# Kernel tuning notes

Measured on AMD Instinct MI355X. Metric: run time of the kernel, lower is better.

Reference implementation:

```python
import jax, jax.numpy as jnp
import numpy as np

B, L, D, K = 16, 2048, 128, 8192
NUM_RQ_STEPS = 1


def _nearest(residual, codebook):
    # residual: [B,L,D], codebook: [K,D]
    d2 = (
        jnp.sum(residual * residual, axis=-1, keepdims=True)  # [B,L,1]
        - 2.0 * jnp.einsum('bld,kd->blk', residual, codebook)  # [B,L,K]
        + jnp.sum(codebook * codebook, axis=-1)  # [K]
    )
    idx = jnp.argmin(d2, axis=-1)  # [B,L]
    return codebook[idx], idx  # gather: [B,L,D]


def setup_inputs() -> dict:
    key = jax.random.key(0)
    k1, k2 = jax.random.split(key)
    z_e = jax.random.normal(k1, (B, L, D), dtype=jnp.float32)
    codebook = jax.random.normal(k2, (K, D), dtype=jnp.float32)
    return {"z_e": z_e, "codebook": codebook}


def reference(z_e, codebook):
    # apply_codebook(z_e, code_sg=True): codebook is stop-gradiented,
    # residual quantization over NUM_RQ_STEPS, straight-through on output.
    cb = jax.lax.stop_gradient(codebook)
    residual = z_e
    z_q = jnp.zeros_like(z_e)
    idx_list = []
    for _ in range(NUM_RQ_STEPS):
        q, idx = _nearest(residual, cb)
        z_q = z_q + q
        residual = residual - q
        idx_list.append(idx)
    indices = jnp.stack(idx_list, axis=-1)  # [B,L,num_rq_steps]
    # straight-through estimator (code_sg=True): grads flow to z_e, not codebook
    z_q = z_e + jax.lax.stop_gradient(z_q - z_e)
    return z_q, indices
```

## Files before the change

kernel.cpp:

```cpp
#include <hip/hip_runtime.h>


#define M_TOK  32768
#define DIM    128
#define KCODES 8192
#define BM     64
#define NT     (KCODES / 256)
#define MARGIN 0.10f

typedef _Float16 half8v __attribute__((ext_vector_type(8)));
typedef float float4v __attribute__((ext_vector_type(4)));

union H2U { _Float16 h; unsigned short u; };
__device__ __forceinline__ unsigned short f2h_bits(_Float16 h) {
  H2U c; c.h = h; return c.u;
}

#define LOADB(bf, base_off) do {                                     \
    _Pragma("unroll") for (int j_ = 0; j_ < 4; ++j_)                 \
      (bf)[j_] = *(const half8v*)(Bp[j_] + (base_off));              \
  } while (0)

#define CONSUME(kk, bf) do {                                         \
    _Pragma("unroll") for (int i_ = 0; i_ < 4; ++i_)                 \
      _Pragma("unroll") for (int j_ = 0; j_ < 4; ++j_)               \
        acc[i_][j_] = __builtin_amdgcn_mfma_f32_16x16x32_f16(        \
            ahi[kk][i_], (bf)[j_], acc[i_][j_], 0, 0, 0);            \
  } while (0)

#define CNORM_OFF  (KCODES * 256)
#define QCNT_OFF   (CNORM_OFF + KCODES * 4)
#define QTOK_OFF   (QCNT_OFF + 64)
#define KMIN_OFF   (QTOK_OFF + M_TOK * 4)

__global__ __launch_bounds__(256) void prep_kernel(
    const float* __restrict__ cb, unsigned short* __restrict__ Cs,
    float* __restrict__ cnorm, int* __restrict__ qcnt) {
  if (blockIdx.x == 0 && threadIdx.x == 0) *qcnt = 0;
  const int k = blockIdx.x * 4 + (threadIdx.x >> 6);
  const int lane = threadIdx.x & 63;
  const float2 v = ((const float2*)(cb + (size_t)k * DIM))[lane];
  float s = v.x * v.x + v.y * v.y;
  #pragma unroll
  for (int off = 32; off > 0; off >>= 1) s += __shfl_down(s, off);
  if (lane == 0) cnorm[k] = s;
  ushort2 hi;
  hi.x = f2h_bits((_Float16)v.x);
  hi.y = f2h_bits((_Float16)v.y);
  *(ushort2*)(Cs + (size_t)k * 128 + lane * 2) = hi;
}

__global__ __launch_bounds__(256, 2) void vq_mfma_kernel(
    const float* __restrict__ ze, const unsigned short* __restrict__ Cs,
    const float* __restrict__ cnorm, const float* __restrict__ cb,
    int* __restrict__ qcnt, int* __restrict__ qtok,
    unsigned long long* __restrict__ kmin,
    float* __restrict__ out_zq, float* __restrict__ out_idx) {
  __shared__ char lds[16384];
  char* const As = lds;

  const int tid = threadIdx.x;
  const int wn = tid >> 6;
  const int lane = tid & 63;
  const int quad = lane >> 4;
  const int l15 = lane & 15;
  const int m0 = blockIdx.x * BM;

  const char* Bp[4];
  #pragma unroll
  for (int j = 0; j < 4; ++j)
    Bp[j] = (const char*)Cs +
            (size_t)(wn * 64 + j * 16 + l15) * 256 + quad * 16;

  {
    const int r = tid >> 2;
    const int qh = tid & 3;
    const float* zrow = ze + (size_t)(m0 + r) * DIM + qh * 32;
    char* arow = As + r * 256;
    const int rx = r & 7;
    #pragma unroll
    for (int i = 0; i < 8; ++i) {
      const float4 v = *(const float4*)(zrow + i * 4);
      ushort4 hh;
      hh.x = f2h_bits((_Float16)v.x);
      hh.y = f2h_bits((_Float16)v.y);
      hh.z = f2h_bits((_Float16)v.z);
      hh.w = f2h_bits((_Float16)v.w);
      const int c = qh * 32 + i * 4;
      *(ushort4*)(arow + ((((c >> 3) ^ rx) << 4) | ((c & 7) << 1))) = hh;
    }
  }
  __syncthreads();

  half8v ahi[4][4];
  #pragma unroll
  for (int ks = 0; ks < 4; ++ks)
    #pragma unroll
    for (int i = 0; i < 4; ++i) {
      const int m = i * 16 + l15;
      const int kslot = ks * 4 + quad;
      ahi[ks][i] = *(const half8v*)(As + m * 256 + ((kslot ^ (m & 7)) << 4));
    }

  float bestv[16], secv[16], idxv[16];
  #pragma unroll
  for (int s = 0; s < 16; ++s) {
    bestv[s] = -3.4e38f; secv[s] = -3.4e38f; idxv[s] = 0.f;
  }

  half8v bf0[4], bf1[4];
  LOADB(bf0, 0);

  for (int nt = 0; nt < NT; ++nt) {
    const size_t tb = (size_t)nt * 65536;
    float cnv[4];
    #pragma unroll
    for (int j = 0; j < 4; ++j)
      cnv[j] = cnorm[nt * 256 + wn * 64 + j * 16 + l15];

    float4v acc[4][4];
    #pragma unroll
    for (int i = 0; i < 4; ++i)
      #pragma unroll
      for (int j = 0; j < 4; ++j) acc[i][j] = (float4v)0.0f;

    LOADB(bf1, tb + 1 * 64);
    CONSUME(0, bf0);
    LOADB(bf0, tb + 2 * 64);
    CONSUME(1, bf1);
    LOADB(bf1, tb + 3 * 64);
    CONSUME(2, bf0);
    if (nt + 1 < NT) LOADB(bf0, tb + 65536);
    CONSUME(3, bf1);

    #pragma unroll
    for (int j = 0; j < 4; ++j) {
      const float nidx = (float)(nt * 256 + wn * 64 + j * 16 + l15);
      const float cn = cnv[j];
      #pragma unroll
      for (int i = 0; i < 4; ++i)
        #pragma unroll
        for (int rg = 0; rg < 4; ++rg) {
          const float sc = fmaf(-0.5f, cn, acc[i][j][rg]);
          const int slot = i * 4 + rg;
          const bool bt = sc > bestv[slot];
          secv[slot] = __builtin_amdgcn_fmed3f(sc, bestv[slot], secv[slot]);
          idxv[slot] = bt ? nidx : idxv[slot];
          bestv[slot] = fmaxf(bestv[slot], sc);
        }
    }
  }

  #pragma unroll
  for (int slot = 0; slot < 16; ++slot) {
    float b = bestv[slot], sec = secv[slot], ix = idxv[slot];
    #pragma unroll
    for (int mk = 1; mk <= 8; mk <<= 1) {
      const float ob = __shfl_xor(b, mk);
      const float os = __shfl_xor(sec, mk);
      const float oi = __shfl_xor(ix, mk);
      const bool take = (ob > b) || (ob == b && oi < ix);
      const float loser = take ? b : ob;
      b = take ? ob : b;
      ix = take ? oi : ix;
      sec = fmaxf(fmaxf(sec, os), loser);
    }
    bestv[slot] = b; secv[slot] = sec; idxv[slot] = ix;
  }

  __syncthreads();
  float* const redB = (float*)lds;
  float* const redS = redB + 256;
  float* const redI = redB + 512;
  float* const lidxs = redB + 768;
  if (l15 == 0) {
    #pragma unroll
    for (int slot = 0; slot < 16; ++slot) {
      const int row = (slot >> 2) * 16 + quad * 4 + (slot & 3);
      redB[wn * 64 + row] = bestv[slot];
      redS[wn * 64 + row] = secv[slot];
      redI[wn * 64 + row] = idxv[slot];
    }
  }
  __syncthreads();
  if (tid < 64) {
    float b = redB[tid], sec = redS[tid], ix = redI[tid];
    #pragma unroll
    for (int w = 1; w < 4; ++w) {
      const float ob = redB[w * 64 + tid];
      const float os = redS[w * 64 + tid];
      const float oi = redI[w * 64 + tid];
      const bool take = (ob > b) || (ob == b && oi < ix);
      const float loser = take ? b : ob;
      b = take ? ob : b;
      ix = take ? oi : ix;
      sec = fmaxf(fmaxf(sec, os), loser);
    }
    out_idx[m0 + tid] = ix;
    lidxs[tid] = ix;
    if (b - sec < 0.5f * MARGIN) {
      kmin[m0 + tid] = ~0ull;
      const int p = atomicAdd(qcnt, 1);
      qtok[p] = m0 + tid;
    }
  }
  __syncthreads();

  const int tl = tid >> 2, qp = tid & 3;
  const int code = (int)lidxs[tl];
  const float4* src = (const float4*)(cb + (size_t)code * DIM);
  float4* dst = (float4*)(out_zq + (size_t)(m0 + tl) * DIM);
  #pragma unroll
  for (int p = 0; p < 8; ++p) dst[qp + p * 4] = src[qp + p * 4];
}

__global__ __launch_bounds__(256) void rescan_part_kernel(
    const float* __restrict__ ze, const float* __restrict__ cb,
    const float* __restrict__ cnorm, const int* __restrict__ qcnt,
    const int* __restrict__ qtok, unsigned long long* __restrict__ kmin) {
  __shared__ float xsh[DIM];
  __shared__ float rs[256];
  __shared__ int ri[256];
  const int tid = threadIdx.x;
  const int chunk = blockIdx.x & 31;
  const int n = *qcnt;
  for (int qi = blockIdx.x >> 5; qi < n; qi += (gridDim.x >> 5)) {
    const int token = qtok[qi];
    __syncthreads();
    if (tid < 32)
      ((float4*)xsh)[tid] = ((const float4*)(ze + (size_t)token * DIM))[tid];
    __syncthreads();
    const int code = chunk * 256 + tid;
    const float* crow = cb + (size_t)code * DIM;
    float dot = 0.f;
    #pragma unroll
    for (int d = 0; d < DIM; ++d) dot = fmaf(xsh[d], crow[d], dot);
    rs[tid] = fmaf(-2.f, dot, cnorm[code]);
    ri[tid] = code;
    __syncthreads();
    #pragma unroll
    for (int off = 128; off > 0; off >>= 1) {
      if (tid < off) {
        const float so = rs[tid + off];
        const int io = ri[tid + off];
        if (so < rs[tid] || (so == rs[tid] && io < ri[tid])) {
          rs[tid] = so; ri[tid] = io;
        }
      }
      __syncthreads();
    }
    if (tid == 0) {
      union { float f; unsigned int u; } c; c.f = rs[0];
      const unsigned int m = (c.u >> 31) ? ~c.u : (c.u | 0x80000000u);
      const unsigned long long key =
          ((unsigned long long)m << 32) | (unsigned int)ri[0];
      atomicMin(&kmin[token], key);
    }
    __syncthreads();
  }
}

__global__ __launch_bounds__(256) void rescan_apply_kernel(
    const float* __restrict__ cb, const int* __restrict__ qcnt,
    const int* __restrict__ qtok, const unsigned long long* __restrict__ kmin,
    float* __restrict__ out_zq, float* __restrict__ out_idx) {
  const int tid = threadIdx.x;
  const int n = *qcnt;
  for (int qi = blockIdx.x; qi < n; qi += gridDim.x) {
    const int token = qtok[qi];
    const int code = (int)(unsigned int)(kmin[token] & 0xFFFFFFFFull);
    if (tid == 0) out_idx[token] = (float)code;
    if (tid < 32)
      ((float4*)(out_zq + (size_t)token * DIM))[tid] =
          ((const float4*)(cb + (size_t)code * DIM))[tid];
  }
}

extern "C" void kernel_launch(void* const* d_in, const int* in_sizes, int n_in,
                              void* d_out, int out_size, void* d_ws,
                              size_t ws_size, hipStream_t stream) {
  const float* ze = (const float*)d_in[0];
  const float* cb = (const float*)d_in[1];
  float* out = (float*)d_out;

  unsigned short* Cs = (unsigned short*)d_ws;
  float* cnorm = (float*)((char*)d_ws + CNORM_OFF);
  int* qcnt = (int*)((char*)d_ws + QCNT_OFF);
  int* qtok = (int*)((char*)d_ws + QTOK_OFF);
  unsigned long long* kmin = (unsigned long long*)((char*)d_ws + KMIN_OFF);

  prep_kernel<<<KCODES / 4, 256, 0, stream>>>(cb, Cs, cnorm, qcnt);
  vq_mfma_kernel<<<M_TOK / BM, 256, 0, stream>>>(
      ze, Cs, cnorm, cb, qcnt, qtok, kmin, out, out + (size_t)M_TOK * DIM);
  rescan_part_kernel<<<4096, 256, 0, stream>>>(ze, cb, cnorm, qcnt, qtok,
                                               kmin);
  rescan_apply_kernel<<<256, 256, 0, stream>>>(cb, qcnt, qtok, kmin, out,
                                               out + (size_t)M_TOK * DIM);
}
```

Before: 295.9 us.

## Split codebook scan into two halves per token tile with separate merge-gather kernel

The main MFMA kernel now processes half of the codebook per block, doubling the grid so twice as many blocks share the token tiles, and raises the occupancy hint to 4 blocks per CU. Per-half best, second-best and index are written to workspace, and a new merge kernel combines them, flags ambiguous tokens for rescan and gathers the codebook rows. This targets low parallelism and tail effects in the 512-block launch. The cost is an extra kernel launch, partial-result traffic through global memory, and A-tile conversion being done twice. Ties between the halves are resolved toward the lower index.

After: 626.8 us. +111.8%, slower.

```diff
diff --git a/kernel.cpp b/kernel.cpp
--- a/kernel.cpp
+++ b/kernel.cpp
@@ -5,7 +5,7 @@
 #define DIM    128
 #define KCODES 8192
 #define BM     64
-#define NT     (KCODES / 256)
+#define NT     16
 #define MARGIN 0.10f
 
 typedef _Float16 half8v __attribute__((ext_vector_type(8)));
@@ -32,6 +32,9 @@
 #define QCNT_OFF   (CNORM_OFF + KCODES * 4)
 #define QTOK_OFF   (QCNT_OFF + 64)
 #define KMIN_OFF   (QTOK_OFF + M_TOK * 4)
+#define PARTB_OFF  (KMIN_OFF + M_TOK * 8)
+#define PARTS_OFF  (PARTB_OFF + M_TOK * 8)
+#define PARTI_OFF  (PARTS_OFF + M_TOK * 8)
 
 __global__ __launch_bounds__(256) void prep_kernel(
     const float* __restrict__ cb, unsigned short* __restrict__ Cs,
@@ -50,12 +53,11 @@
   *(ushort2*)(Cs + (size_t)k * 128 + lane * 2) = hi;
 }
 
-__global__ __launch_bounds__(256, 2) void vq_mfma_kernel(
+__global__ __launch_bounds__(256, 4) void vq_mfma_kernel(
     const float* __restrict__ ze, const unsigned short* __restrict__ Cs,
-    const float* __restrict__ cnorm, const float* __restrict__ cb,
-    int* __restrict__ qcnt, int* __restrict__ qtok,
-    unsigned long long* __restrict__ kmin,
-    float* __restrict__ out_zq, float* __restrict__ out_idx) {
+    const float* __restrict__ cnorm,
+    float* __restrict__ partB, float* __restrict__ partS,
+    float* __restrict__ partI) {
   __shared__ char lds[16384];
   char* const As = lds;
 
@@ -64,13 +66,15 @@
   const int lane = tid & 63;
   const int quad = lane >> 4;
   const int l15 = lane & 15;
-  const int m0 = blockIdx.x * BM;
+  const int m0 = (blockIdx.x >> 1) * BM;
+  const int kh = blockIdx.x & 1;
+  const int cbase = kh * 4096;
 
   const char* Bp[4];
   #pragma unroll
   for (int j = 0; j < 4; ++j)
     Bp[j] = (const char*)Cs +
-            (size_t)(wn * 64 + j * 16 + l15) * 256 + quad * 16;
+            (size_t)(cbase + wn * 64 + j * 16 + l15) * 256 + quad * 16;
 
   {
     const int r = tid >> 2;
@@ -116,7 +120,7 @@
     float cnv[4];
     #pragma unroll
     for (int j = 0; j < 4; ++j)
-      cnv[j] = cnorm[nt * 256 + wn * 64 + j * 16 + l15];
+      cnv[j] = cnorm[cbase + nt * 256 + wn * 64 + j * 16 + l15];
 
     float4v acc[4][4];
     #pragma unroll
@@ -135,7 +139,7 @@
 
     #pragma unroll
     for (int j = 0; j < 4; ++j) {
-      const float nidx = (float)(nt * 256 + wn * 64 + j * 16 + l15);
+      const float nidx = (float)(cbase + nt * 256 + wn * 64 + j * 16 + l15);
       const float cn = cnv[j];
       #pragma unroll
       for (int i = 0; i < 4; ++i)
@@ -172,7 +176,6 @@
   float* const redB = (float*)lds;
   float* const redS = redB + 256;
   float* const redI = redB + 512;
-  float* const lidxs = redB + 768;
   if (l15 == 0) {
     #pragma unroll
     for (int slot = 0; slot < 16; ++slot) {
@@ -196,22 +199,47 @@
       ix = take ? oi : ix;
       sec = fmaxf(fmaxf(sec, os), loser);
     }
-    out_idx[m0 + tid] = ix;
-    lidxs[tid] = ix;
+    const int token = m0 + tid;
+    partB[token * 2 + kh] = b;
+    partS[token * 2 + kh] = sec;
+    partI[token * 2 + kh] = ix;
+  }
+}
+
+__global__ __launch_bounds__(256) void merge_gather_kernel(
+    const float* __restrict__ cb,
+    const float* __restrict__ partB, const float* __restrict__ partS,
+    const float* __restrict__ partI,
+    int* __restrict__ qcnt, int* __restrict__ qtok,
+    unsigned long long* __restrict__ kmin,
+    float* __restrict__ out_zq, float* __restrict__ out_idx) {
+  __shared__ float lidx[32];
+  const int tid = threadIdx.x;
+  const int t0 = blockIdx.x * 32;
+  if (tid < 32) {
+    const int token = t0 + tid;
+    const float b0 = partB[token * 2 + 0], b1 = partB[token * 2 + 1];
+    const float s0 = partS[token * 2 + 0], s1 = partS[token * 2 + 1];
+    const float i0 = partI[token * 2 + 0], i1 = partI[token * 2 + 1];
+    const bool take = b1 > b0;
+    const float b = take ? b1 : b0;
+    const float ix = take ? i1 : i0;
+    const float sec = fmaxf(fminf(b0, b1), fmaxf(s0, s1));
+    out_idx[token] = ix;
+    lidx[tid] = ix;
     if (b - sec < 0.5f * MARGIN) {
-      kmin[m0 + tid] = ~0ull;
+      kmin[token] = ~0ull;
       const int p = atomicAdd(qcnt, 1);
-      qtok[p] = m0 + tid;
+      qtok[p] = token;
     }
   }
   __syncthreads();
-
-  const int tl = tid >> 2, qp = tid & 3;
-  const int code = (int)lidxs[tl];
+  const int tl = tid >> 3, qp = tid & 7;
+  const int code = (int)lidx[tl];
   const float4* src = (const float4*)(cb + (size_t)code * DIM);
-  float4* dst = (float4*)(out_zq + (size_t)(m0 + tl) * DIM);
-  #pragma unroll
-  for (int p = 0; p < 8; ++p) dst[qp + p * 4] = src[qp + p * 4];
+  float4* dst = (float4*)(out_zq + (size_t)(t0 + tl) * DIM);
+  #pragma unroll
+  for (int p = 0; p < 4; ++p) dst[qp + p * 8] = src[qp + p * 8];
 }
 
 __global__ __launch_bounds__(256) void rescan_part_kernel(
@@ -288,10 +316,16 @@
   int* qcnt = (int*)((char*)d_ws + QCNT_OFF);
   int* qtok = (int*)((char*)d_ws + QTOK_OFF);
   unsigned long long* kmin = (unsigned long long*)((char*)d_ws + KMIN_OFF);
+  float* partB = (float*)((char*)d_ws + PARTB_OFF);
+  float* partS = (float*)((char*)d_ws + PARTS_OFF);
+  float* partI = (float*)((char*)d_ws + PARTI_OFF);
 
   prep_kernel<<<KCODES / 4, 256, 0, stream>>>(cb, Cs, cnorm, qcnt);
-  vq_mfma_kernel<<<M_TOK / BM, 256, 0, stream>>>(
-      ze, Cs, cnorm, cb, qcnt, qtok, kmin, out, out + (size_t)M_TOK * DIM);
+  vq_mfma_kernel<<<(M_TOK / BM) * 2, 256, 0, stream>>>(
+      ze, Cs, cnorm, partB, partS, partI);
+  merge_gather_kernel<<<M_TOK / 32, 256, 0, stream>>>(
+      cb, partB, partS, partI, qcnt, qtok, kmin, out,
+      out + (size_t)M_TOK * DIM);
   rescan_part_kernel<<<4096, 256, 0, stream>>>(ze, cb, cnorm, qcnt, qtok,
                                                kmin);
   rescan_apply_kernel<<<256, 256, 0, stream>>>(cb, qcnt, qtok, kmin, out,
```
